# Performance work log

Measured on AMD Instinct MI355X. Metric: run time of the kernel, lower is better.

## Reference

```python
import jax, jax.numpy as jnp
import numpy as np

H = 1024      # hidden_size
L = 2         # num_layers
B = 4096      # batch_size (acts as sequential time axis)
IN = 33       # LSTM input size (17 raw + 8 ip-embed + 8 port-embed)


def setup_inputs() -> dict:
    key = jax.random.key(0)
    ks = jax.random.split(key, 16)
    s = 0.02
    return {
        "x": jax.random.normal(ks[0], (B, 17), dtype=jnp.float32),
        "ip": jax.random.randint(ks[1], (B, 8), 0, 256),
        "port": jax.random.randint(ks[2], (B, 2), 0, 70000),
        "hidden": jnp.zeros((L, 1, H), dtype=jnp.float32),
        "cell": jnp.zeros((L, 1, H), dtype=jnp.float32),
        "ip_emb": jax.random.normal(ks[3], (256, 1), dtype=jnp.float32) * s,
        "port_emb": jax.random.normal(ks[4], (70000, 4), dtype=jnp.float32) * s,
        "W_ih0": jax.random.normal(ks[5], (4 * H, IN), dtype=jnp.float32) * s,
        "W_hh0": jax.random.normal(ks[6], (4 * H, H), dtype=jnp.float32) * s,
        "b_ih0": jax.random.normal(ks[7], (4 * H,), dtype=jnp.float32) * s,
        "b_hh0": jax.random.normal(ks[8], (4 * H,), dtype=jnp.float32) * s,
        "W_ih1": jax.random.normal(ks[9], (4 * H, H), dtype=jnp.float32) * s,
        "W_hh1": jax.random.normal(ks[10], (4 * H, H), dtype=jnp.float32) * s,
        "b_ih1": jax.random.normal(ks[11], (4 * H,), dtype=jnp.float32) * s,
        "b_hh1": jax.random.normal(ks[12], (4 * H,), dtype=jnp.float32) * s,
    }


def reference(x, ip, port, hidden, cell, ip_emb, port_emb,
              W_ih0, W_hh0, b_ih0, b_hh0, W_ih1, W_hh1, b_ih1, b_hh1):
    # embedding lookups + concat -> [B, 33]
    ip_e = ip_emb[ip].reshape(B, -1)        # [B, 8]
    port_e = port_emb[port].reshape(B, -1)  # [B, 8]
    xin = jnp.concatenate((x, ip_e, port_e), axis=1)  # [B, 33]

    Wih = (W_ih0, W_ih1)
    Whh = (W_hh0, W_hh1)
    bih = (b_ih0, b_ih1)
    bhh = (b_hh0, b_hh1)

    h0 = hidden[:, 0]  # [L, H]
    c0 = cell[:, 0]    # [L, H]

    def step(carry, xt):
        h, c = carry
        inp = xt
        hs, cs = [], []
        for l in range(L):  # fixed small layer loop
            gates = Wih[l] @ inp + bih[l] + Whh[l] @ h[l] + bhh[l]  # [4H]
            i, f, g, o = jnp.split(gates, 4)  # PyTorch gate order: i,f,g,o
            i = jax.nn.sigmoid(i)
            f = jax.nn.sigmoid(f)
            g = jnp.tanh(g)
            o = jax.nn.sigmoid(o)
            c_new = f * c[l] + i * g
            h_new = o * jnp.tanh(c_new)
            hs.append(h_new)
            cs.append(c_new)
            inp = h_new
        return (jnp.stack(hs), jnp.stack(cs)), jax.nn.relu(inp)

    (hf, cf), outputs = jax.lax.scan(step, (h0, c0), xin)
    return outputs, (hf[:, None, :], cf[:, None, :])
```

## Files before the change

kernel.cpp:

```cpp
#include <hip/hip_runtime.h>
#include <hip/hip_fp16.h>
#include <math.h>

#define Hn 1024
#define Bn 4096
#define INW 33
#define OUTS (Bn * Hn)
#define TPB 512
#define ROWP 1024

typedef _Float16 half2v __attribute__((ext_vector_type(2)));
typedef unsigned uint4v __attribute__((ext_vector_type(4)));

__device__ __forceinline__ float sigmoidf_(float x) {
    return 1.0f / (1.0f + __expf(-x));
}
__device__ __forceinline__ float tanhf_(float x) {
    float e = __expf(-2.0f * fabsf(x));
    float r = (1.0f - e) / (1.0f + e);
    return copysignf(r, x);
}
__device__ __forceinline__ unsigned pack2(float a, float b) {
    __half2 h = __floats2half2_rn(a, b);
    return __builtin_bit_cast(unsigned, h);
}
__device__ __forceinline__ float dot2acc(unsigned w, unsigned hv, float acc) {
#if __has_builtin(__builtin_amdgcn_fdot2)
    return __builtin_amdgcn_fdot2(__builtin_bit_cast(half2v, w),
                                  __builtin_bit_cast(half2v, hv), acc, false);
#else
    __half2 wh = __builtin_bit_cast(__half2, w);
    __half2 hh = __builtin_bit_cast(__half2, hv);
    float2 wf = __half22float2(wh), hf = __half22float2(hh);
    return acc + wf.x * hf.x + wf.y * hf.y;
#endif
}

__device__ __forceinline__ void probe_spin(const unsigned long long* p, unsigned tag) {
    int rounds = 0;
    for (;;) {
        unsigned long long v;
        asm volatile("global_load_dwordx2 %0, %1, off sc0 sc1\n\t"
                     "s_waitcnt vmcnt(0)"
                     : "=v"(v) : "v"(p) : "memory");
        if ((unsigned)(v >> 32) == tag) break;
        if (++rounds > (1 << 24)) break;
    }
}

__device__ __forceinline__ void poll_row(const unsigned long long* halfbase, int lane,
                                         unsigned tag, uint4v& r0, uint4v& r1,
                                         uint4v& r2, uint4v& r3) {
    const char* p = (const char*)halfbase + lane * 16;
    int rounds = 0;
    for (;;) {
        asm volatile(
            "global_load_dwordx4 %0, %4, off sc0 sc1\n\t"
            "global_load_dwordx4 %1, %4, off offset:1024 sc0 sc1\n\t"
            "global_load_dwordx4 %2, %4, off offset:2048 sc0 sc1\n\t"
            "global_load_dwordx4 %3, %4, off offset:3072 sc0 sc1\n\t"
            "s_waitcnt vmcnt(0)"
            : "=v"(r0), "=v"(r1), "=v"(r2), "=v"(r3)
            : "v"(p)
            : "memory");
        bool ok = (r0.y == tag) & (r0.w == tag) & (r1.y == tag) & (r1.w == tag)
                & (r2.y == tag) & (r2.w == tag) & (r3.y == tag) & (r3.w == tag);
        if (__all(ok)) break;
        if (++rounds > (1 << 22)) break;
    }
}

__device__ __forceinline__ void row_to_lds(unsigned* hs2, int base, int lane,
                                           const uint4v& r0, const uint4v& r1,
                                           const uint4v& r2, const uint4v& r3) {
    hs2[base +       2 * lane]     = r0.x;  hs2[base +       2 * lane + 1] = r0.z;
    hs2[base + 128 + 2 * lane]     = r1.x;  hs2[base + 128 + 2 * lane + 1] = r1.z;
    hs2[base + 256 + 2 * lane]     = r2.x;  hs2[base + 256 + 2 * lane + 1] = r2.z;
    hs2[base + 384 + 2 * lane]     = r3.x;  hs2[base + 384 + 2 * lane + 1] = r3.z;
}

__device__ __forceinline__ void store16_coherent(void* dst, uint4v v) {
    asm volatile("global_store_dwordx4 %0, %1, off sc0 sc1"
                 :: "v"(dst), "v"(v) : "memory");
}

__global__ void prep_kernel(const float* __restrict__ x, const int* __restrict__ ip,
                            const int* __restrict__ port, const float* __restrict__ ip_emb,
                            const float* __restrict__ port_emb, float* __restrict__ xin) {
    int gid = blockIdx.x * blockDim.x + threadIdx.x;
    if (gid < Bn * INW) {
        int t = gid / INW;
        int k = gid - t * INW;
        float v;
        if (k < 17) {
            v = x[t * 17 + k];
        } else if (k < 25) {
            v = ip_emb[ip[t * 8 + (k - 17)]];
        } else {
            int kk = k - 25;
            v = port_emb[port[t * 2 + (kk >> 2)] * 4 + (kk & 3)];
        }
        xin[gid] = v;
    }
}

__global__ void __launch_bounds__(TPB, 2) lstm_kernel(
    const float* __restrict__ xin,
    const float* __restrict__ hid0, const float* __restrict__ cel0,
    const float* __restrict__ Wih0, const float* __restrict__ Whh0,
    const float* __restrict__ bih0, const float* __restrict__ bhh0,
    const float* __restrict__ Wih1, const float* __restrict__ Whh1,
    const float* __restrict__ bih1, const float* __restrict__ bhh1,
    float* __restrict__ out,
    unsigned long long* __restrict__ rowpkt)
{
    __shared__ unsigned hs2[1024];
    __shared__ unsigned long long stg[16];
    const int tid  = threadIdx.x;
    const int lane = tid & 63;
    const int wave = tid >> 6;
    const int bx   = blockIdx.x;

    if (bx < 32) {
        const int j0 = bx * 32 + wave * 4;
        const int probe0 = (bx * 67 + 13) & 511;
        unsigned w2[4][4][8];
        float    wx[4][4];
        float    bs[4][4];
#pragma unroll
        for (int jj = 0; jj < 4; ++jj) {
#pragma unroll
            for (int g = 0; g < 4; ++g) {
                const int row = g * Hn + (j0 + jj);
                const float* wr = Whh0 + (size_t)row * Hn;
#pragma unroll
                for (int k = 0; k < 8; ++k) {
                    int c = lane + 64 * k;
                    w2[jj][g][k] = pack2(wr[2 * c], wr[2 * c + 1]);
                }
                wx[jj][g] = (lane < INW) ? Wih0[row * INW + lane] : 0.0f;
                bs[jj][g] = bih0[row] + bhh0[row];
            }
        }
        float cst[4], hcur[4];
#pragma unroll
        for (int jj = 0; jj < 4; ++jj) { cst[jj] = cel0[j0 + jj]; hcur[jj] = 0.0f; }

        for (int s = 0; s < Bn; ++s) {
            float xv = xin[s * INW + (lane < INW ? lane : 0)];
            if (wave == 0) {
                if (s == 0) {
#pragma unroll
                    for (int m = 0; m < 8; ++m) {
                        int q = lane + 64 * m;
                        hs2[q] = pack2(hid0[2 * q], hid0[2 * q + 1]);
                    }
                } else {
                    const unsigned long long* rb = rowpkt + (size_t)(s - 1) * ROWP;
                    probe_spin(rb + probe0, (unsigned)s);
                    uint4v r0, r1, r2, r3;
                    poll_row(rb, lane, (unsigned)s, r0, r1, r2, r3);
                    row_to_lds(hs2, 0, lane, r0, r1, r2, r3);
                }
            }
            __syncthreads();

            float acc[4][4];
#pragma unroll
            for (int jj = 0; jj < 4; ++jj)
#pragma unroll
                for (int g = 0; g < 4; ++g) acc[jj][g] = wx[jj][g] * xv;
#pragma unroll
            for (int k = 0; k < 8; ++k) {
                unsigned hv = hs2[lane + 64 * k];
#pragma unroll
                for (int jj = 0; jj < 4; ++jj)
#pragma unroll
                    for (int g = 0; g < 4; ++g)
                        acc[jj][g] = dot2acc(w2[jj][g][k], hv, acc[jj][g]);
            }
            __syncthreads();

#pragma unroll
            for (int off = 32; off >= 1; off >>= 1)
#pragma unroll
                for (int jj = 0; jj < 4; ++jj)
#pragma unroll
                    for (int g = 0; g < 4; ++g)
                        acc[jj][g] += __shfl_xor(acc[jj][g], off);

#pragma unroll
            for (int jj = 0; jj < 4; ++jj) {
                float gi = sigmoidf_(acc[jj][0] + bs[jj][0]);
                float gf = sigmoidf_(acc[jj][1] + bs[jj][1]);
                float gg = tanhf_   (acc[jj][2] + bs[jj][2]);
                float go = sigmoidf_(acc[jj][3] + bs[jj][3]);
                cst[jj] = gf * cst[jj] + gi * gg;
                hcur[jj] = go * tanhf_(cst[jj]);
            }
            if (lane == 0) {
                unsigned long long tw = ((unsigned long long)(s + 1)) << 32;
                stg[2 * wave]     = tw | pack2(hcur[0], hcur[1]);
                stg[2 * wave + 1] = tw | pack2(hcur[2], hcur[3]);
            }
            __syncthreads();
            if (wave == 0 && lane < 8) {
                uint4v v = *(const uint4v*)&stg[2 * lane];
                char* dst = (char*)(rowpkt + (size_t)s * ROWP) + bx * 128 + lane * 16;
                store16_coherent(dst, v);
            }
        }
        if (lane == 0) {
#pragma unroll
            for (int jj = 0; jj < 4; ++jj) {
                out[OUTS + j0 + jj] = hcur[jj];
                out[OUTS + 2 * Hn + j0 + jj] = cst[jj];
            }
        }
    } else {
        const int blk = bx - 32;
        const int j0  = blk * 16 + wave * 2;
        const int probeA = ((blk + 64) * 67 + 13) & 511;
        const int probeB = 512 + ((blk * 67 + 13) & 511);
        unsigned w2[2][4][16];
        float    bs[2][4];
#pragma unroll
        for (int jj = 0; jj < 2; ++jj) {
#pragma unroll
            for (int g = 0; g < 4; ++g) {
                const int row = g * Hn + (j0 + jj);
                const float* wr1 = Wih1 + (size_t)row * Hn;
                const float* wr2 = Whh1 + (size_t)row * Hn;
#pragma unroll
                for (int k = 0; k < 8; ++k) {
                    int c = lane + 64 * k;
                    w2[jj][g][k]     = pack2(wr1[2 * c], wr1[2 * c + 1]);
                    w2[jj][g][8 + k] = pack2(wr2[2 * c], wr2[2 * c + 1]);
                }
                bs[jj][g] = bih1[row] + bhh1[row];
            }
        }
        float cst[2], hcur[2];
#pragma unroll
        for (int jj = 0; jj < 2; ++jj) { cst[jj] = cel0[Hn + j0 + jj]; hcur[jj] = 0.0f; }

        if (lane == 0)
            stg[wave] = (1ULL << 32) | pack2(hid0[Hn + j0], hid0[Hn + j0 + 1]);
        __syncthreads();
        if (wave == 0 && lane < 4) {
            uint4v v = *(const uint4v*)&stg[2 * lane];
            char* dst = (char*)(rowpkt + 512) + blk * 64 + lane * 16;
            store16_coherent(dst, v);
        }

        for (int s = 1; s <= Bn; ++s) {
            const int t = s - 1;
            const unsigned long long* rb = rowpkt + (size_t)(s - 1) * ROWP;
            if (wave == 0) {
                probe_spin(rb + probeA, (unsigned)s);
                uint4v r0, r1, r2, r3;
                poll_row(rb, lane, (unsigned)s, r0, r1, r2, r3);
                row_to_lds(hs2, 0, lane, r0, r1, r2, r3);
            } else if (wave == 1) {
                probe_spin(rb + probeB, (unsigned)s);
                uint4v r0, r1, r2, r3;
                poll_row(rb + 512, lane, (unsigned)s, r0, r1, r2, r3);
                row_to_lds(hs2, 512, lane, r0, r1, r2, r3);
            }
            __syncthreads();

            float acc[2][4];
#pragma unroll
            for (int jj = 0; jj < 2; ++jj)
#pragma unroll
                for (int g = 0; g < 4; ++g) acc[jj][g] = 0.0f;
#pragma unroll
            for (int k = 0; k < 16; ++k) {
                unsigned hv = hs2[lane + 64 * k];
#pragma unroll
                for (int jj = 0; jj < 2; ++jj)
#pragma unroll
                    for (int g = 0; g < 4; ++g)
                        acc[jj][g] = dot2acc(w2[jj][g][k], hv, acc[jj][g]);
            }
            __syncthreads();

#pragma unroll
            for (int off = 32; off >= 1; off >>= 1)
#pragma unroll
                for (int jj = 0; jj < 2; ++jj)
#pragma unroll
                    for (int g = 0; g < 4; ++g)
                        acc[jj][g] += __shfl_xor(acc[jj][g], off);

#pragma unroll
            for (int jj = 0; jj < 2; ++jj) {
                float gi = sigmoidf_(acc[jj][0] + bs[jj][0]);
                float gf = sigmoidf_(acc[jj][1] + bs[jj][1]);
                float gg = tanhf_   (acc[jj][2] + bs[jj][2]);
                float go = sigmoidf_(acc[jj][3] + bs[jj][3]);
                cst[jj] = gf * cst[jj] + gi * gg;
                hcur[jj] = go * tanhf_(cst[jj]);
            }
            if (lane == 0) {
                unsigned long long tw = ((unsigned long long)(s + 1)) << 32;
                stg[wave] = tw | pack2(hcur[0], hcur[1]);
                float2 o2 = make_float2(fmaxf(hcur[0], 0.0f), fmaxf(hcur[1], 0.0f));
                *(float2*)(out + (size_t)t * Hn + j0) = o2;
            }
            __syncthreads();
            if (wave == 0 && lane < 4) {
                uint4v v = *(const uint4v*)&stg[2 * lane];
                char* dst = (char*)(rowpkt + (size_t)s * ROWP + 512) + blk * 64 + lane * 16;
                store16_coherent(dst, v);
            }
        }
        if (lane == 0) {
#pragma unroll
            for (int jj = 0; jj < 2; ++jj) {
                out[OUTS + Hn + j0 + jj] = hcur[jj];
                out[OUTS + 3 * Hn + j0 + jj] = cst[jj];
            }
        }
    }
}

extern "C" void kernel_launch(void* const* d_in, const int* in_sizes, int n_in,
                              void* d_out, int out_size, void* d_ws, size_t ws_size,
                              hipStream_t stream) {
    const float* x        = (const float*)d_in[0];
    const int*   ip       = (const int*)d_in[1];
    const int*   port     = (const int*)d_in[2];
    const float* hidden   = (const float*)d_in[3];
    const float* cell     = (const float*)d_in[4];
    const float* ip_emb   = (const float*)d_in[5];
    const float* port_emb = (const float*)d_in[6];
    const float* Wih0     = (const float*)d_in[7];
    const float* Whh0     = (const float*)d_in[8];
    const float* bih0     = (const float*)d_in[9];
    const float* bhh0     = (const float*)d_in[10];
    const float* Wih1     = (const float*)d_in[11];
    const float* Whh1     = (const float*)d_in[12];
    const float* bih1     = (const float*)d_in[13];
    const float* bhh1     = (const float*)d_in[14];
    float* out = (float*)d_out;

    unsigned long long* rowpkt = (unsigned long long*)d_ws;
    float* xin = (float*)(rowpkt + (size_t)(Bn + 1) * ROWP);

    prep_kernel<<<dim3((Bn * INW + 255) / 256), dim3(256), 0, stream>>>(
        x, ip, port, ip_emb, port_emb, xin);

    lstm_kernel<<<dim3(96), dim3(TPB), 0, stream>>>(
        xin, hidden, cell, Wih0, Whh0, bih0, bhh0, Wih1, Whh1, bih1, bhh1,
        out, rowpkt);
}
```

Baseline: 17.23 ms.

## Halve block count, poll row slices per wave, double-buffer LDS to drop a barrier

Blocks grow from 512 to 1024 threads, so 48 blocks replace 96 and each handles twice as many hidden units. Instead of one wave probing and then polling the whole row packet, every wave spins on its own 64-entry slice and writes the result straight into LDS. The hidden-state LDS buffer is double-buffered by step parity, which removes the barrier that followed the dot products. The aim is to shorten the per-timestep cross-block handoff latency, at the cost of higher per-block register pressure and more polling traffic.

```diff
diff --git a/kernel.cpp b/kernel.cpp
--- a/kernel.cpp
+++ b/kernel.cpp
@@ -6,7 +6,6 @@
 #define Bn 4096
 #define INW 33
 #define OUTS (Bn * Hn)
-#define TPB 512
 #define ROWP 1024
 
 typedef _Float16 half2v __attribute__((ext_vector_type(2)));
@@ -36,47 +35,18 @@
 #endif
 }
 
-__device__ __forceinline__ void probe_spin(const unsigned long long* p, unsigned tag) {
+__device__ __forceinline__ unsigned spin_slice(const unsigned long long* slice,
+                                               int lane, unsigned tag) {
+    unsigned long long v;
     int rounds = 0;
     for (;;) {
-        unsigned long long v;
         asm volatile("global_load_dwordx2 %0, %1, off sc0 sc1\n\t"
                      "s_waitcnt vmcnt(0)"
-                     : "=v"(v) : "v"(p) : "memory");
-        if ((unsigned)(v >> 32) == tag) break;
+                     : "=v"(v) : "v"(slice + lane) : "memory");
+        if (__all((unsigned)(v >> 32) == tag)) break;
         if (++rounds > (1 << 24)) break;
     }
-}
-
-__device__ __forceinline__ void poll_row(const unsigned long long* halfbase, int lane,
-                                         unsigned tag, uint4v& r0, uint4v& r1,
-                                         uint4v& r2, uint4v& r3) {
-    const char* p = (const char*)halfbase + lane * 16;
-    int rounds = 0;
-    for (;;) {
-        asm volatile(
-            "global_load_dwordx4 %0, %4, off sc0 sc1\n\t"
-            "global_load_dwordx4 %1, %4, off offset:1024 sc0 sc1\n\t"
-            "global_load_dwordx4 %2, %4, off offset:2048 sc0 sc1\n\t"
-            "global_load_dwordx4 %3, %4, off offset:3072 sc0 sc1\n\t"
-            "s_waitcnt vmcnt(0)"
-            : "=v"(r0), "=v"(r1), "=v"(r2), "=v"(r3)
-            : "v"(p)
-            : "memory");
-        bool ok = (r0.y == tag) & (r0.w == tag) & (r1.y == tag) & (r1.w == tag)
-                & (r2.y == tag) & (r2.w == tag) & (r3.y == tag) & (r3.w == tag);
-        if (__all(ok)) break;
-        if (++rounds > (1 << 22)) break;
-    }
-}
-
-__device__ __forceinline__ void row_to_lds(unsigned* hs2, int base, int lane,
-                                           const uint4v& r0, const uint4v& r1,
-                                           const uint4v& r2, const uint4v& r3) {
-    hs2[base +       2 * lane]     = r0.x;  hs2[base +       2 * lane + 1] = r0.z;
-    hs2[base + 128 + 2 * lane]     = r1.x;  hs2[base + 128 + 2 * lane + 1] = r1.z;
-    hs2[base + 256 + 2 * lane]     = r2.x;  hs2[base + 256 + 2 * lane + 1] = r2.z;
-    hs2[base + 384 + 2 * lane]     = r3.x;  hs2[base + 384 + 2 * lane + 1] = r3.z;
+    return (unsigned)v;
 }
 
 __device__ __forceinline__ void store16_coherent(void* dst, uint4v v) {
@@ -104,7 +74,7 @@
     }
 }
 
-__global__ void __launch_bounds__(TPB, 2) lstm_kernel(
+__global__ void __launch_bounds__(1024, 2) lstm_kernel(
     const float* __restrict__ xin,
     const float* __restrict__ hid0, const float* __restrict__ cel0,
     const float* __restrict__ Wih0, const float* __restrict__ Whh0,
@@ -114,16 +84,15 @@
     float* __restrict__ out,
     unsigned long long* __restrict__ rowpkt)
 {
-    __shared__ unsigned hs2[1024];
-    __shared__ unsigned long long stg[16];
+    __shared__ unsigned hs2[2][1024];
+    __shared__ unsigned long long stg[32];
     const int tid  = threadIdx.x;
     const int lane = tid & 63;
     const int wave = tid >> 6;
     const int bx   = blockIdx.x;
 
-    if (bx < 32) {
-        const int j0 = bx * 32 + wave * 4;
-        const int probe0 = (bx * 67 + 13) & 511;
+    if (bx < 16) {
+        const int j0 = bx * 64 + wave * 4;
         unsigned w2[4][4][8];
         float    wx[4][4];
         float    bs[4][4];
@@ -147,20 +116,16 @@
         for (int jj = 0; jj < 4; ++jj) { cst[jj] = cel0[j0 + jj]; hcur[jj] = 0.0f; }
 
         for (int s = 0; s < Bn; ++s) {
+            const int b = s & 1;
             float xv = xin[s * INW + (lane < INW ? lane : 0)];
-            if (wave == 0) {
+            if (wave < 8) {
                 if (s == 0) {
-#pragma unroll
-                    for (int m = 0; m < 8; ++m) {
-                        int q = lane + 64 * m;
-                        hs2[q] = pack2(hid0[2 * q], hid0[2 * q + 1]);
-                    }
+                    int q = wave * 64 + lane;
+                    hs2[0][q] = pack2(hid0[2 * q], hid0[2 * q + 1]);
                 } else {
-                    const unsigned long long* rb = rowpkt + (size_t)(s - 1) * ROWP;
-                    probe_spin(rb + probe0, (unsigned)s);
-                    uint4v r0, r1, r2, r3;
-                    poll_row(rb, lane, (unsigned)s, r0, r1, r2, r3);
-                    row_to_lds(hs2, 0, lane, r0, r1, r2, r3);
+                    unsigned d = spin_slice(rowpkt + (size_t)(s - 1) * ROWP + wave * 64,
+                                            lane, (unsigned)s);
+                    hs2[b][wave * 64 + lane] = d;
                 }
             }
             __syncthreads();
@@ -172,14 +137,13 @@
                 for (int g = 0; g < 4; ++g) acc[jj][g] = wx[jj][g] * xv;
 #pragma unroll
             for (int k = 0; k < 8; ++k) {
-                unsigned hv = hs2[lane + 64 * k];
+                unsigned hv = hs2[b][lane + 64 * k];
 #pragma unroll
                 for (int jj = 0; jj < 4; ++jj)
 #pragma unroll
                     for (int g = 0; g < 4; ++g)
                         acc[jj][g] = dot2acc(w2[jj][g][k], hv, acc[jj][g]);
             }
-            __syncthreads();
 
 #pragma unroll
             for (int off = 32; off >= 1; off >>= 1)
@@ -204,9 +168,9 @@
                 stg[2 * wave + 1] = tw | pack2(hcur[2], hcur[3]);
             }
             __syncthreads();
-            if (wave == 0 && lane < 8) {
+            if (wave == 0 && lane < 16) {
                 uint4v v = *(const uint4v*)&stg[2 * lane];
-                char* dst = (char*)(rowpkt + (size_t)s * ROWP) + bx * 128 + lane * 16;
+                char* dst = (char*)(rowpkt + (size_t)s * ROWP) + bx * 256 + lane * 16;
                 store16_coherent(dst, v);
             }
         }
@@ -218,10 +182,8 @@
             }
         }
     } else {
-        const int blk = bx - 32;
-        const int j0  = blk * 16 + wave * 2;
-        const int probeA = ((blk + 64) * 67 + 13) & 511;
-        const int probeB = 512 + ((blk * 67 + 13) & 511);
+        const int blk = bx - 16;
+        const int j0  = blk * 32 + wave * 2;
         unsigned w2[2][4][16];
         float    bs[2][4];
 #pragma unroll
@@ -244,29 +206,21 @@
 #pragma unroll
         for (int jj = 0; jj < 2; ++jj) { cst[jj] = cel0[Hn + j0 + jj]; hcur[jj] = 0.0f; }
 
-        if (lane == 0)
-            stg[wave] = (1ULL << 32) | pack2(hid0[Hn + j0], hid0[Hn + j0 + 1]);
-        __syncthreads();
-        if (wave == 0 && lane < 4) {
-            uint4v v = *(const uint4v*)&stg[2 * lane];
-            char* dst = (char*)(rowpkt + 512) + blk * 64 + lane * 16;
+        if (wave == 0 && lane < 8) {
+            int base = Hn + blk * 32 + 4 * lane;
+            uint4v v;
+            v.x = pack2(hid0[base],     hid0[base + 1]);  v.y = 1u;
+            v.z = pack2(hid0[base + 2], hid0[base + 3]);  v.w = 1u;
+            char* dst = (char*)(rowpkt + 512) + blk * 128 + lane * 16;
             store16_coherent(dst, v);
         }
 
         for (int s = 1; s <= Bn; ++s) {
             const int t = s - 1;
-            const unsigned long long* rb = rowpkt + (size_t)(s - 1) * ROWP;
-            if (wave == 0) {
-                probe_spin(rb + probeA, (unsigned)s);
-                uint4v r0, r1, r2, r3;
-                poll_row(rb, lane, (unsigned)s, r0, r1, r2, r3);
-                row_to_lds(hs2, 0, lane, r0, r1, r2, r3);
-            } else if (wave == 1) {
-                probe_spin(rb + probeB, (unsigned)s);
-                uint4v r0, r1, r2, r3;
-                poll_row(rb + 512, lane, (unsigned)s, r0, r1, r2, r3);
-                row_to_lds(hs2, 512, lane, r0, r1, r2, r3);
-            }
+            const int b = s & 1;
+            unsigned d = spin_slice(rowpkt + (size_t)(s - 1) * ROWP + wave * 64,
+                                    lane, (unsigned)s);
+            hs2[b][wave * 64 + lane] = d;
             __syncthreads();
 
             float acc[2][4];
@@ -276,14 +230,13 @@
                 for (int g = 0; g < 4; ++g) acc[jj][g] = 0.0f;
 #pragma unroll
             for (int k = 0; k < 16; ++k) {
-                unsigned hv = hs2[lane + 64 * k];
+                unsigned hv = hs2[b][lane + 64 * k];
 #pragma unroll
                 for (int jj = 0; jj < 2; ++jj)
 #pragma unroll
                     for (int g = 0; g < 4; ++g)
                         acc[jj][g] = dot2acc(w2[jj][g][k], hv, acc[jj][g]);
             }
-            __syncthreads();
 
 #pragma unroll
             for (int off = 32; off >= 1; off >>= 1)
@@ -309,9 +262,9 @@
                 *(float2*)(out + (size_t)t * Hn + j0) = o2;
             }
             __syncthreads();
-            if (wave == 0 && lane < 4) {
+            if (wave == 0 && lane < 8) {
                 uint4v v = *(const uint4v*)&stg[2 * lane];
-                char* dst = (char*)(rowpkt + (size_t)s * ROWP + 512) + blk * 64 + lane * 16;
+                char* dst = (char*)(rowpkt + (size_t)s * ROWP + 512) + blk * 128 + lane * 16;
                 store16_coherent(dst, v);
             }
         }
@@ -351,7 +304,7 @@
     prep_kernel<<<dim3((Bn * INW + 255) / 256), dim3(256), 0, stream>>>(
         x, ip, port, ip_emb, port_emb, xin);
 
-    lstm_kernel<<<dim3(96), dim3(TPB), 0, stream>>>(
+    lstm_kernel<<<dim3(48), dim3(1024), 0, stream>>>(
         xin, hidden, cell, Wih0, Whh0, bih0, bhh0, Wih1, Whh1, bih1, bhh1,
         out, rowpkt);
 }
```

Result: slower. 51.56 ms (+199.3%).
